# Optimization experiments

Measured on AMD Instinct MI355X. Metric: run time of the kernel, lower is better.

The kernel has to match this reference:

```python
import jax, jax.numpy as jnp
import numpy as np

B, P, N, De, H, Do, T = 256, 48, 64, 64, 128, 64, 5
NR = N * (N - 1)
EPS = 1e-5


def _w(k, o, i):
    return jax.random.normal(k, (o, i), jnp.float32) * (1.0 / np.sqrt(i))


def setup_inputs() -> dict:
    key = jax.random.key(0)
    ks = jax.random.split(key, 12)
    x = jax.random.normal(ks[0], (B, P, N), jnp.float32)
    # fully-connected directed edges without self-loops (order matches itertools.product)
    idx = np.array([(r, s) for r in range(N) for s in range(N) if r != s], dtype=np.int32)
    receivers = jnp.asarray(idx[:, 0])
    senders = jnp.asarray(idx[:, 1])
    inp = {
        "x": x,
        "receivers": receivers,
        "senders": senders,
        "bn_gamma": jnp.ones((P,), jnp.float32),
        "bn_beta": jnp.zeros((P,), jnp.float32),
        "fr1_w": _w(ks[1], 4 * De, 2 * P), "fr1_b": jnp.zeros((4 * De,), jnp.float32),
        "fr2_w": _w(ks[2], 2 * De, 4 * De), "fr2_b": jnp.zeros((2 * De,), jnp.float32),
        "fr3_w": _w(ks[3], De, 2 * De), "fr3_b": jnp.zeros((De,), jnp.float32),
        "fo1_w": _w(ks[4], 2 * H, P + De), "fo1_b": jnp.zeros((2 * H,), jnp.float32),
        "fo2_w": _w(ks[5], H, 2 * H), "fo2_b": jnp.zeros((H,), jnp.float32),
        "fo3_w": _w(ks[6], Do, H), "fo3_b": jnp.zeros((Do,), jnp.float32),
        "fc1_w": _w(ks[7], 5 * T, Do), "fc1_b": jnp.zeros((5 * T,), jnp.float32),
        "fc2_w": _w(ks[8], 3 * T, 5 * T), "fc2_b": jnp.zeros((3 * T,), jnp.float32),
        "fc3_w": _w(ks[9], T, 3 * T), "fc3_b": jnp.zeros((T,), jnp.float32),
    }
    return inp


def _conv1(x, w, b):  # 1x1 Conv1d: x [B,Cin,L], w [Cout,Cin]
    return jnp.einsum('oi,bil->bol', w, x) + b[None, :, None]


def _forward(x, receivers, senders, bn_gamma, bn_beta,
             fr1_w, fr1_b, fr2_w, fr2_b, fr3_w, fr3_b,
             fo1_w, fo1_b, fo2_w, fo2_b, fo3_w, fo3_b,
             fc1_w, fc1_b, fc2_w, fc2_b, fc3_w, fc3_b):
    relu = jax.nn.relu
    # BatchNorm1d(P) in training mode: stats over (batch, length)
    mean = jnp.mean(x, axis=(0, 2), keepdims=True)
    var = jnp.var(x, axis=(0, 2), keepdims=True)
    xn = (x - mean) * jax.lax.rsqrt(var + EPS)
    xn = xn * bn_gamma[None, :, None] + bn_beta[None, :, None]
    # tmul(x, Rr)/tmul(x, Rs) are one-hot gathers along node axis -> [B, P, Nr]
    Orr = xn[:, :, receivers]
    Ors = xn[:, :, senders]
    Bmat = jnp.concatenate([Orr, Ors], axis=1)  # [B, 2P, Nr]
    Bmat = relu(_conv1(Bmat, fr1_w, fr1_b))
    Bmat = relu(_conv1(Bmat, fr2_w, fr2_b))
    E = relu(_conv1(Bmat, fr3_w, fr3_b))  # [B, De, Nr]
    # tmul(E, Rr^T) is scatter-add of edge features onto receiver nodes
    Ebar = jnp.zeros((x.shape[0], De, N), E.dtype).at[:, :, receivers].add(E)
    C = jnp.concatenate([xn, Ebar], axis=1)  # [B, P+De, N]
    C = relu(_conv1(C, fo1_w, fo1_b))
    C = relu(_conv1(C, fo2_w, fo2_b))
    O = relu(_conv1(C, fo3_w, fo3_b))  # [B, Do, N]
    Nsum = jnp.sum(O, axis=2)  # sum over constituents -> [B, Do]
    # fc_fixed1/2/3 applied with NO intermediate activations
    out = Nsum @ fc1_w.T + fc1_b
    out = out @ fc2_w.T + fc2_b
    out = out @ fc3_w.T + fc3_b
    return out


def reference(x, receivers, senders, bn_gamma, bn_beta,
              fr1_w, fr1_b, fr2_w, fr2_b, fr3_w, fr3_b,
              fo1_w, fo1_b, fo2_w, fo2_b, fo3_w, fo3_b,
              fc1_w, fc1_b, fc2_w, fc2_b, fc3_w, fc3_b):
    return _forward(x, receivers, senders, bn_gamma, bn_beta,
                    fr1_w, fr1_b, fr2_w, fr2_b, fr3_w, fr3_b,
                    fo1_w, fo1_b, fo2_w, fo2_b, fo3_w, fo3_b,
                    fc1_w, fc1_b, fc2_w, fc2_b, fc3_w, fc3_b)
```

## Files before the change

### kernel.cpp

```cpp
#include <hip/hip_runtime.h>
#include <hip/hip_fp16.h>

#define BB 256
#define PP 48
#define NN 64
#define EPSBN 1e-5f

typedef __attribute__((ext_vector_type(8))) short sh8;
typedef __attribute__((ext_vector_type(8))) _Float16 f16x8;
typedef __attribute__((ext_vector_type(4))) float f32x4;
typedef __attribute__((ext_vector_type(2))) _Float16 f16x2;
typedef __attribute__((ext_vector_type(2))) __fp16 fp16v2;

#define BIGO 0
#define S1SO 32768
#define S1RO 49152
#define F3LO 65536
#define A2WO 73728
#define XNTP 73728
#define B2LO 81408
#define REDO 81664
#define LDSE 81920

#define W_FR1R 0
#define W_FR1S 16384
#define W_FR2  32768
#define W_FR3  65536
#define W_FO1  73728
#define W_FO2  106496
#define W_FO3  139264
#define W_TOT  147456
#define W_XNT  147456
#define W_ALL  (W_XNT + BB * 4096)

union U8 { sh8 v; unsigned u[4]; };
union H2U { unsigned u; f16x2 f; fp16v2 p; };

__device__ __forceinline__ unsigned pkh(float a, float b) {
    H2U c; c.p = __builtin_amdgcn_cvt_pkrtz(a, b);
    return c.u;
}
__device__ __forceinline__ ushort f2h(float f) {
    union { _Float16 h; ushort s; } c; c.h = (_Float16)f;
    return c.s;
}
__device__ __forceinline__ unsigned reluAddH2(unsigned a, unsigned b) {
    H2U x, y, r;
    x.u = a; y.u = b;
    f16x2 s = x.f + y.f;
    f16x2 z = {(_Float16)0.f, (_Float16)0.f};
    r.f = __builtin_elementwise_max(s, z);
    return r.u;
}

__device__ __forceinline__ int sidx(int row, int k, int kpad) {
    return row * kpad + ((((k >> 3) ^ (row & 7)) << 3) | (k & 7));
}
__device__ __forceinline__ sh8 ldfrag(const ushort* buf, int row, int k, int kpad) {
    return *(const sh8*)(buf + row * kpad + (((k >> 3) ^ (row & 7)) << 3));
}
__device__ __forceinline__ sh8 ldfrag40(const ushort* buf, int row, int k) {
    return *(const sh8*)(buf + row * 40 + k);
}
__device__ __forceinline__ f32x4 MFMA(sh8 a, sh8 b, f32x4 c) {
    union { sh8 s; f16x8 f; } ca, cb;
    ca.s = a; cb.s = b;
    return __builtin_amdgcn_mfma_f32_16x16x32_f16(ca.f, cb.f, c, 0, 0, 0);
}
__device__ __forceinline__ void stAct(ushort* buf, int row, int c0, int kpad, f32x4 a, float4 bi) {
    uint2 o;
    o.x = pkh(fmaxf(a[0] + bi.x, 0.f), fmaxf(a[1] + bi.y, 0.f));
    o.y = pkh(fmaxf(a[2] + bi.z, 0.f), fmaxf(a[3] + bi.w, 0.f));
    *(uint2*)(buf + row * kpad + ((((c0 >> 3) ^ (row & 7)) << 3) | (c0 & 7))) = o;
}
__device__ __forceinline__ void stAct040(ushort* buf, int row, int c0, f32x4 a) {
    uint2 o;
    o.x = pkh(fmaxf(a[0], 0.f), fmaxf(a[1], 0.f));
    o.y = pkh(fmaxf(a[2], 0.f), fmaxf(a[3], 0.f));
    *(uint2*)(buf + row * 40 + c0) = o;
}
__device__ __forceinline__ void stRaw(ushort* buf, int row, int c0, int kpad, f32x4 a, float4 bi) {
    uint2 o;
    o.x = pkh(a[0] + bi.x, a[1] + bi.y);
    o.y = pkh(a[2] + bi.z, a[3] + bi.w);
    *(uint2*)(buf + row * kpad + ((((c0 >> 3) ^ (row & 7)) << 3) | (c0 & 7))) = o;
}

__global__ __launch_bounds__(1024) void bn_stats_kernel(
    const float* __restrict__ x, const float* __restrict__ gamma,
    const float* __restrict__ beta, float* __restrict__ scale, float* __restrict__ bias)
{
    __shared__ float s_sum[1024], s_sq[1024];
    int p = blockIdx.x, t = threadIdx.x;
    float sum = 0.f, sq = 0.f;
    for (int i = t; i < BB * NN; i += 1024) {
        int b = i >> 6, n = i & 63;
        float v = x[b * PP * NN + p * NN + n];
        sum += v; sq += v * v;
    }
    s_sum[t] = sum; s_sq[t] = sq;
    __syncthreads();
    for (int off = 512; off > 0; off >>= 1) {
        if (t < off) { s_sum[t] += s_sum[t + off]; s_sq[t] += s_sq[t + off]; }
        __syncthreads();
    }
    if (t == 0) {
        float inv = 1.f / (float)(BB * NN);
        float mean = s_sum[0] * inv;
        float var  = s_sq[0] * inv - mean * mean;
        float sc   = gamma[p] * rsqrtf(var + EPSBN);
        scale[p] = sc;
        bias[p]  = beta[p] - mean * sc;
    }
}

__global__ __launch_bounds__(512) void prep_kernel(
    const float* __restrict__ fr1_w, const float* __restrict__ fr2_w,
    const float* __restrict__ fr3_w, const float* __restrict__ fo1_w,
    const float* __restrict__ fo2_w, const float* __restrict__ fo3_w,
    const float* __restrict__ x, const float* __restrict__ scale,
    const float* __restrict__ bias, ushort* __restrict__ wsw)
{
    int i = blockIdx.x * 512 + threadIdx.x;
    if (i >= W_ALL) return;
    if (i >= W_TOT) {
        int j = i - W_XNT;
        int b = j >> 12, nk = j & 4095, n = nk & 63, k = nk >> 6;
        float v = (k < PP) ? x[b * PP * NN + k * NN + n] * scale[k] + bias[k] : 0.f;
        wsw[W_XNT + (b << 12) + sidx(n, k, 64)] = f2h(v);
        return;
    }
    float v; int off, row, k, kpad;
    if (i < 16384)        { row = i >> 6; k = i & 63; kpad = 64;  off = W_FR1R;
                            v = (k < PP) ? fr1_w[row * 96 + k] : 0.f; }
    else if (i < 32768)   { int j = i - 16384;  row = j >> 6; k = j & 63;  kpad = 64;  off = W_FR1S;
                            v = (k < PP) ? fr1_w[row * 96 + PP + k] : 0.f; }
    else if (i < 65536)   { int j = i - 32768;  row = j >> 8; k = j & 255; kpad = 256; off = W_FR2;
                            v = fr2_w[row * 256 + k]; }
    else if (i < 73728)   { int j = i - 65536;  row = j >> 7; k = j & 127; kpad = 128; off = W_FR3;
                            v = fr3_w[row * 128 + k]; }
    else if (i < 106496)  { int j = i - 73728;  row = j >> 7; k = j & 127; kpad = 128; off = W_FO1;
                            v = (k < 64) ? fo1_w[row * 112 + PP + k]
                              : (k < 112 ? fo1_w[row * 112 + (k - 64)] : 0.f); }
    else if (i < 139264)  { int j = i - 106496; row = j >> 8; k = j & 255; kpad = 256; off = W_FO2;
                            v = fo2_w[row * 256 + k]; }
    else                  { int j = i - 139264; row = j >> 7; k = j & 127; kpad = 128; off = W_FO3;
                            v = fo3_w[row * 128 + k]; }
    wsw[off + sidx(row, k, kpad)] = f2h(v);
}

__device__ __forceinline__ void wcopy(ushort* dst, const ushort* src, int n, int t) {
    for (int i = t * 8; i < n; i += 768 * 8)
        *(uint4*)(dst + i) = *(const uint4*)(src + i);
}

__global__ __launch_bounds__(768, 3) void meg_kernel(
    const ushort* __restrict__ wsw,
    const float* __restrict__ fr1_b, const float* __restrict__ fr2_b,
    const float* __restrict__ fr3_b, const float* __restrict__ fo1_b,
    const float* __restrict__ fo2_b, const float* __restrict__ fo3_b,
    const float* __restrict__ fc1_w, const float* __restrict__ fc1_b,
    const float* __restrict__ fc2_w, const float* __restrict__ fc2_b,
    const float* __restrict__ fc3_w, const float* __restrict__ fc3_b,
    float* __restrict__ out)
{
    __shared__ __align__(16) ushort L[LDSE];

    int b = blockIdx.x, t = threadIdx.x;
    int w = t >> 6, l = t & 63, lx = l & 15, lq = l >> 4;

    wcopy(L + XNTP,         wsw + W_XNT + (b << 12), 4096, t);
    wcopy(L + BIGO,         wsw + W_FR1R, 16384, t);
    wcopy(L + BIGO + 16384, wsw + W_FR1S, 16384, t);
    wcopy(L + F3LO,         wsw + W_FR3,  8192, t);
    if (t < 128) ((float*)(L + B2LO))[t] = fr2_b[t];
    __syncthreads();

    for (int mt = w; mt < 16; mt += 12) {
        f32x4 aR[4], aS[4];
#pragma unroll
        for (int nt = 0; nt < 4; ++nt) { aR[nt] = (f32x4){0.f,0.f,0.f,0.f}; aS[nt] = (f32x4){0.f,0.f,0.f,0.f}; }
#pragma unroll
        for (int ks = 0; ks < 2; ++ks) {
            sh8 AfR = ldfrag(L + BIGO,         mt * 16 + lx, ks * 32 + lq * 8, 64);
            sh8 AfS = ldfrag(L + BIGO + 16384, mt * 16 + lx, ks * 32 + lq * 8, 64);
#pragma unroll
            for (int nt = 0; nt < 4; ++nt) {
                sh8 Bf = ldfrag(L + XNTP, nt * 16 + lx, ks * 32 + lq * 8, 64);
                aR[nt] = MFMA(AfR, Bf, aR[nt]);
                aS[nt] = MFMA(AfS, Bf, aS[nt]);
            }
        }
        int ch0 = mt * 16 + lq * 4;
        float4 bi = *(const float4*)(fr1_b + ch0);
        float4 zb = make_float4(0.f, 0.f, 0.f, 0.f);
#pragma unroll
        for (int nt = 0; nt < 4; ++nt) {
            stRaw(L + S1RO, nt * 16 + lx, ch0, 256, aR[nt], bi);
            stRaw(L + S1SO, nt * 16 + lx, ch0, 256, aS[nt], zb);
        }
    }
    __syncthreads();

    wcopy(L + BIGO, wsw + W_FR2, 32768, t);
    float b3c[4];
#pragma unroll
    for (int n3 = 0; n3 < 4; ++n3) b3c[n3] = fr3_b[n3 * 16 + lx];
    __syncthreads();

    ushort* a2w = L + A2WO + w * 640;
    const float* b2L = (const float*)(L + B2LO);
#pragma unroll 1
    for (int r = w; r < 64; r += 12) {
        float part[4] = {0.f, 0.f, 0.f, 0.f};
#pragma unroll 1
        for (int p = 0; p < 2; ++p) {
            int eA = p * 32 + lx, eB = eA + 16;
            int sA = eA + (eA >= r);
            int sB = eB + (eB >= r); if (sB > 63) sB = 63;

            f32x4 acc2[8][2];
#pragma unroll
            for (int m = 0; m < 8; ++m) {
                float4 bv = *(const float4*)(b2L + m * 16 + lq * 4);
                f32x4 bi; bi[0] = bv.x; bi[1] = bv.y; bi[2] = bv.z; bi[3] = bv.w;
                acc2[m][0] = bi; acc2[m][1] = bi;
            }
#pragma unroll
            for (int ks = 0; ks < 8; ++ks) {
                int ko = ks * 32 + lq * 8;
                U8 fr, fa, fb;
                fr.v = ldfrag(L + S1RO, r,  ko, 256);
                fa.v = ldfrag(L + S1SO, sA, ko, 256);
                fb.v = ldfrag(L + S1SO, sB, ko, 256);
                U8 bA, bB;
#pragma unroll
                for (int jj = 0; jj < 4; ++jj) {
                    bA.u[jj] = reluAddH2(fr.u[jj], fa.u[jj]);
                    bB.u[jj] = reluAddH2(fr.u[jj], fb.u[jj]);
                }
#pragma unroll
                for (int m = 0; m < 8; ++m) {
                    sh8 Af = ldfrag(L + BIGO, m * 16 + lx, ko, 256);
                    acc2[m][0] = MFMA(Af, bA.v, acc2[m][0]);
                    acc2[m][1] = MFMA(Af, bB.v, acc2[m][1]);
                }
            }
            f32x4 acc3[2][4];
#pragma unroll
            for (int cc = 0; cc < 2; ++cc)
#pragma unroll
                for (int n3 = 0; n3 < 4; ++n3) acc3[cc][n3] = (f32x4){0.f,0.f,0.f,0.f};
#pragma unroll
            for (int h = 0; h < 4; ++h) {
                sh8 bW[4];
#pragma unroll
                for (int n3 = 0; n3 < 4; ++n3)
                    bW[n3] = ldfrag(L + F3LO, n3 * 16 + lx, h * 32 + lq * 8, 128);
#pragma unroll
                for (int cc = 0; cc < 2; ++cc) {
                    stAct040(a2w, lx, lq * 4,      acc2[2 * h][cc]);
                    stAct040(a2w, lx, 16 + lq * 4, acc2[2 * h + 1][cc]);
                    sh8 af = ldfrag40(a2w, lx, lq * 8);
#pragma unroll
                    for (int n3 = 0; n3 < 4; ++n3)
                        acc3[cc][n3] = MFMA(af, bW[n3], acc3[cc][n3]);
                }
            }
#pragma unroll
            for (int cc = 0; cc < 2; ++cc) {
                bool mpad = (p == 1) && (cc == 1) && (lq == 3);
#pragma unroll
                for (int n3 = 0; n3 < 4; ++n3) {
                    float bv = b3c[n3];
                    float s = fmaxf(acc3[cc][n3][0] + bv, 0.f) + fmaxf(acc3[cc][n3][1] + bv, 0.f)
                            + fmaxf(acc3[cc][n3][2] + bv, 0.f);
                    float s3 = fmaxf(acc3[cc][n3][3] + bv, 0.f);
                    part[n3] += s + (mpad ? 0.f : s3);
                }
            }
        }
#pragma unroll
        for (int n3 = 0; n3 < 4; ++n3) {
            part[n3] += __shfl_xor(part[n3], 16, 64);
            part[n3] += __shfl_xor(part[n3], 32, 64);
        }
        if (lq == 0) {
#pragma unroll
            for (int n3 = 0; n3 < 4; ++n3)
                L[S1RO + sidx(r, n3 * 16 + lx, 256)] = f2h(part[n3]);
        }
    }
    __syncthreads();

    wcopy(L + BIGO, wsw + W_FO1, 32768, t);
    wcopy(L + XNTP, wsw + W_XNT + (b << 12), 4096, t);
    __syncthreads();

    for (int mt = w; mt < 16; mt += 12) {
        f32x4 accN[4];
#pragma unroll
        for (int nt = 0; nt < 4; ++nt) accN[nt] = (f32x4){0.f,0.f,0.f,0.f};
#pragma unroll
        for (int ks = 0; ks < 4; ++ks) {
            sh8 Af = ldfrag(L + BIGO, mt * 16 + lx, ks * 32 + lq * 8, 128);
#pragma unroll
            for (int nt = 0; nt < 4; ++nt) {
                sh8 Bf = (ks < 2) ? ldfrag(L + S1RO, nt * 16 + lx, ks * 32 + lq * 8, 256)
                                  : ldfrag(L + XNTP, nt * 16 + lx, (ks - 2) * 32 + lq * 8, 64);
                accN[nt] = MFMA(Af, Bf, accN[nt]);
            }
        }
        int ch0 = mt * 16 + lq * 4;
        float4 bi = *(const float4*)(fo1_b + ch0);
#pragma unroll
        for (int nt = 0; nt < 4; ++nt)
            stAct(L + S1SO, nt * 16 + lx, ch0, 256, accN[nt], bi);
    }
    __syncthreads();

    wcopy(L + BIGO, wsw + W_FO2, 32768, t);
    wcopy(L + S1RO, wsw + W_FO3, 8192, t);
    __syncthreads();

    if (w < 8) {
        f32x4 a2N[4];
#pragma unroll
        for (int nt = 0; nt < 4; ++nt) a2N[nt] = (f32x4){0.f,0.f,0.f,0.f};
#pragma unroll
        for (int ks = 0; ks < 8; ++ks) {
            sh8 Af = ldfrag(L + BIGO, w * 16 + lx, ks * 32 + lq * 8, 256);
#pragma unroll
            for (int nt = 0; nt < 4; ++nt) {
                sh8 Bf = ldfrag(L + S1SO, nt * 16 + lx, ks * 32 + lq * 8, 256);
                a2N[nt] = MFMA(Af, Bf, a2N[nt]);
            }
        }
        int ch0 = w * 16 + lq * 4;
        float4 bi = *(const float4*)(fo2_b + ch0);
#pragma unroll
        for (int nt = 0; nt < 4; ++nt)
            stAct(L + F3LO, nt * 16 + lx, ch0, 128, a2N[nt], bi);
    }
    __syncthreads();

    if (w < 4) {
        f32x4 a3N[4];
#pragma unroll
        for (int nt = 0; nt < 4; ++nt) a3N[nt] = (f32x4){0.f,0.f,0.f,0.f};
#pragma unroll
        for (int ks3 = 0; ks3 < 4; ++ks3) {
            sh8 Af = ldfrag(L + S1RO, 16 * w + lx, ks3 * 32 + lq * 8, 128);
#pragma unroll
            for (int nt = 0; nt < 4; ++nt) {
                sh8 Bf = ldfrag(L + F3LO, nt * 16 + lx, ks3 * 32 + lq * 8, 128);
                a3N[nt] = MFMA(Af, Bf, a3N[nt]);
            }
        }
        float4 b3 = *(const float4*)(fo3_b + 16 * w + lq * 4);
        float o0 = 0.f, o1 = 0.f, o2 = 0.f, o3 = 0.f;
#pragma unroll
        for (int nt = 0; nt < 4; ++nt) {
            o0 += fmaxf(a3N[nt][0] + b3.x, 0.f);
            o1 += fmaxf(a3N[nt][1] + b3.y, 0.f);
            o2 += fmaxf(a3N[nt][2] + b3.z, 0.f);
            o3 += fmaxf(a3N[nt][3] + b3.w, 0.f);
        }
#pragma unroll
        for (int off = 8; off >= 1; off >>= 1) {
            o0 += __shfl_xor(o0, off, 16);
            o1 += __shfl_xor(o1, off, 16);
            o2 += __shfl_xor(o2, off, 16);
            o3 += __shfl_xor(o3, off, 16);
        }
        if (lx == 0) {
            float* red = (float*)(L + REDO);
            *(float4*)&red[16 * w + lq * 4] = make_float4(o0, o1, o2, o3);
        }
    }
    __syncthreads();

    {
        float* red = (float*)(L + REDO);
        float* h1  = red + 64;
        float* h2  = red + 96;
        for (int o = w; o < 25; o += 12) {
            float v = fc1_w[o * 64 + l] * red[l];
#pragma unroll
            for (int off = 32; off >= 1; off >>= 1) v += __shfl_xor(v, off, 64);
            if (l == 0) h1[o] = v + fc1_b[o];
        }
        __syncthreads();
        for (int o = w; o < 15; o += 12) {
            float v = (l < 25) ? fc2_w[o * 25 + l] * h1[l] : 0.f;
#pragma unroll
            for (int off = 32; off >= 1; off >>= 1) v += __shfl_xor(v, off, 64);
            if (l == 0) h2[o] = v + fc2_b[o];
        }
        __syncthreads();
        if (w < 5) {
            float v = (l < 15) ? fc3_w[w * 15 + l] * h2[l] : 0.f;
#pragma unroll
            for (int off = 32; off >= 1; off >>= 1) v += __shfl_xor(v, off, 64);
            if (l == 0) out[b * 5 + w] = v + fc3_b[w];
        }
    }
}

extern "C" void kernel_launch(void* const* d_in, const int* in_sizes, int n_in,
                              void* d_out, int out_size, void* d_ws, size_t ws_size,
                              hipStream_t stream)
{
    const float* x        = (const float*)d_in[0];
    const float* bn_gamma = (const float*)d_in[3];
    const float* bn_beta  = (const float*)d_in[4];
    const float* fr1_w = (const float*)d_in[5];
    const float* fr1_b = (const float*)d_in[6];
    const float* fr2_w = (const float*)d_in[7];
    const float* fr2_b = (const float*)d_in[8];
    const float* fr3_w = (const float*)d_in[9];
    const float* fr3_b = (const float*)d_in[10];
    const float* fo1_w = (const float*)d_in[11];
    const float* fo1_b = (const float*)d_in[12];
    const float* fo2_w = (const float*)d_in[13];
    const float* fo2_b = (const float*)d_in[14];
    const float* fo3_w = (const float*)d_in[15];
    const float* fo3_b = (const float*)d_in[16];
    const float* fc1_w = (const float*)d_in[17];
    const float* fc1_b = (const float*)d_in[18];
    const float* fc2_w = (const float*)d_in[19];
    const float* fc2_b = (const float*)d_in[20];
    const float* fc3_w = (const float*)d_in[21];
    const float* fc3_b = (const float*)d_in[22];

    float* ws    = (float*)d_ws;
    float* scale = ws;
    float* bias  = ws + 64;
    ushort* wsw  = (ushort*)(ws + 128);
    float* out   = (float*)d_out;

    bn_stats_kernel<<<dim3(PP), dim3(1024), 0, stream>>>(x, bn_gamma, bn_beta, scale, bias);
    prep_kernel<<<dim3(W_ALL / 512), dim3(512), 0, stream>>>(
        fr1_w, fr2_w, fr3_w, fo1_w, fo2_w, fo3_w, x, scale, bias, wsw);
    meg_kernel<<<dim3(BB), dim3(768), 0, stream>>>(
        wsw,
        fr1_b, fr2_b, fr3_b, fo1_b, fo2_b, fo3_b,
        fc1_w, fc1_b, fc2_w, fc2_b, fc3_w, fc3_b, out);
}
```

Before: 206.8 us.

## Merge BN stats with weight prep and normalize input inside main kernel

Combines the batch-norm statistics kernel and the weight-swizzle kernel into one launch, with separate block ranges for each job, removing one kernel launch. The normalized, transposed fp16 input is no longer staged through global workspace. The main kernel instead reads x directly, applies the BN scale and bias, and writes it swizzled into LDS, and it does this in two places. This saves a launch and a global round trip, at the cost of redundant conversion work and strided fp32 loads in the main kernel.

```diff
diff --git a/kernel.cpp b/kernel.cpp
--- a/kernel.cpp
+++ b/kernel.cpp
@@ -30,8 +30,6 @@
 #define W_FO2  106496
 #define W_FO3  139264
 #define W_TOT  147456
-#define W_XNT  147456
-#define W_ALL  (W_XNT + BB * 4096)
 
 union U8 { sh8 v; unsigned u[4]; };
 union H2U { unsigned u; f16x2 f; fp16v2 p; };
@@ -86,50 +84,42 @@
     *(uint2*)(buf + row * kpad + ((((c0 >> 3) ^ (row & 7)) << 3) | (c0 & 7))) = o;
 }
 
-__global__ __launch_bounds__(1024) void bn_stats_kernel(
+__global__ __launch_bounds__(1024) void bnprep_kernel(
     const float* __restrict__ x, const float* __restrict__ gamma,
-    const float* __restrict__ beta, float* __restrict__ scale, float* __restrict__ bias)
-{
-    __shared__ float s_sum[1024], s_sq[1024];
-    int p = blockIdx.x, t = threadIdx.x;
-    float sum = 0.f, sq = 0.f;
-    for (int i = t; i < BB * NN; i += 1024) {
-        int b = i >> 6, n = i & 63;
-        float v = x[b * PP * NN + p * NN + n];
-        sum += v; sq += v * v;
-    }
-    s_sum[t] = sum; s_sq[t] = sq;
-    __syncthreads();
-    for (int off = 512; off > 0; off >>= 1) {
-        if (t < off) { s_sum[t] += s_sum[t + off]; s_sq[t] += s_sq[t + off]; }
-        __syncthreads();
-    }
-    if (t == 0) {
-        float inv = 1.f / (float)(BB * NN);
-        float mean = s_sum[0] * inv;
-        float var  = s_sq[0] * inv - mean * mean;
-        float sc   = gamma[p] * rsqrtf(var + EPSBN);
-        scale[p] = sc;
-        bias[p]  = beta[p] - mean * sc;
-    }
-}
-
-__global__ __launch_bounds__(512) void prep_kernel(
+    const float* __restrict__ beta, float* __restrict__ scale, float* __restrict__ bias,
     const float* __restrict__ fr1_w, const float* __restrict__ fr2_w,
     const float* __restrict__ fr3_w, const float* __restrict__ fo1_w,
     const float* __restrict__ fo2_w, const float* __restrict__ fo3_w,
-    const float* __restrict__ x, const float* __restrict__ scale,
-    const float* __restrict__ bias, ushort* __restrict__ wsw)
+    ushort* __restrict__ wsw)
 {
-    int i = blockIdx.x * 512 + threadIdx.x;
-    if (i >= W_ALL) return;
-    if (i >= W_TOT) {
-        int j = i - W_XNT;
-        int b = j >> 12, nk = j & 4095, n = nk & 63, k = nk >> 6;
-        float v = (k < PP) ? x[b * PP * NN + k * NN + n] * scale[k] + bias[k] : 0.f;
-        wsw[W_XNT + (b << 12) + sidx(n, k, 64)] = f2h(v);
+    __shared__ float s_sum[1024], s_sq[1024];
+    int t = threadIdx.x;
+    if (blockIdx.x < PP) {
+        int p = blockIdx.x;
+        float sum = 0.f, sq = 0.f;
+        for (int i = t; i < BB * NN; i += 1024) {
+            int b = i >> 6, n = i & 63;
+            float v = x[b * PP * NN + p * NN + n];
+            sum += v; sq += v * v;
+        }
+        s_sum[t] = sum; s_sq[t] = sq;
+        __syncthreads();
+        for (int off = 512; off > 0; off >>= 1) {
+            if (t < off) { s_sum[t] += s_sum[t + off]; s_sq[t] += s_sq[t + off]; }
+            __syncthreads();
+        }
+        if (t == 0) {
+            float inv = 1.f / (float)(BB * NN);
+            float mean = s_sum[0] * inv;
+            float var  = s_sq[0] * inv - mean * mean;
+            float sc   = gamma[p] * rsqrtf(var + EPSBN);
+            scale[p] = sc;
+            bias[p]  = beta[p] - mean * sc;
+        }
         return;
     }
+    int i = (blockIdx.x - PP) * 1024 + t;
+    if (i >= W_TOT) return;
     float v; int off, row, k, kpad;
     if (i < 16384)        { row = i >> 6; k = i & 63; kpad = 64;  off = W_FR1R;
                             v = (k < PP) ? fr1_w[row * 96 + k] : 0.f; }
@@ -155,6 +145,8 @@
 }
 
 __global__ __launch_bounds__(768, 3) void meg_kernel(
+    const float* __restrict__ x,
+    const float* __restrict__ scl, const float* __restrict__ bia,
     const ushort* __restrict__ wsw,
     const float* __restrict__ fr1_b, const float* __restrict__ fr2_b,
     const float* __restrict__ fr3_b, const float* __restrict__ fo1_b,
@@ -169,7 +161,11 @@
     int b = blockIdx.x, t = threadIdx.x;
     int w = t >> 6, l = t & 63, lx = l & 15, lq = l >> 4;
 
-    wcopy(L + XNTP,         wsw + W_XNT + (b << 12), 4096, t);
+    for (int i = t; i < 4096; i += 768) {
+        int n = i & 63, k = i >> 6;
+        float v = (k < PP) ? x[b * PP * NN + k * NN + n] * scl[k] + bia[k] : 0.f;
+        L[XNTP + sidx(n, k, 64)] = f2h(v);
+    }
     wcopy(L + BIGO,         wsw + W_FR1R, 16384, t);
     wcopy(L + BIGO + 16384, wsw + W_FR1S, 16384, t);
     wcopy(L + F3LO,         wsw + W_FR3,  8192, t);
@@ -294,7 +290,11 @@
     __syncthreads();
 
     wcopy(L + BIGO, wsw + W_FO1, 32768, t);
-    wcopy(L + XNTP, wsw + W_XNT + (b << 12), 4096, t);
+    for (int i = t; i < 4096; i += 768) {
+        int n = i & 63, k = i >> 6;
+        float v = (k < PP) ? x[b * PP * NN + k * NN + n] * scl[k] + bia[k] : 0.f;
+        L[XNTP + sidx(n, k, 64)] = f2h(v);
+    }
     __syncthreads();
 
     for (int mt = w; mt < 16; mt += 12) {
@@ -439,11 +439,11 @@
     ushort* wsw  = (ushort*)(ws + 128);
     float* out   = (float*)d_out;
 
-    bn_stats_kernel<<<dim3(PP), dim3(1024), 0, stream>>>(x, bn_gamma, bn_beta, scale, bias);
-    prep_kernel<<<dim3(W_ALL / 512), dim3(512), 0, stream>>>(
-        fr1_w, fr2_w, fr3_w, fo1_w, fo2_w, fo3_w, x, scale, bias, wsw);
+    bnprep_kernel<<<dim3(PP + W_TOT / 1024), dim3(1024), 0, stream>>>(
+        x, bn_gamma, bn_beta, scale, bias,
+        fr1_w, fr2_w, fr3_w, fo1_w, fo2_w, fo3_w, wsw);
     meg_kernel<<<dim3(BB), dim3(768), 0, stream>>>(
-        wsw,
+        x, scale, bias, wsw,
         fr1_b, fr2_b, fr3_b, fo1_b, fo2_b, fo3_b,
         fc1_w, fc1_b, fc2_w, fc2_b, fc3_w, fc3_b, out);
 }
```

After: 203.5 us. Within noise of the previous version (-1.6%).
